# Performance work log

Measured on AMD Instinct MI355X. Metric: run time of the kernel, lower is better.

Reference implementation:

```python
import jax, jax.numpy as jnp
import numpy as np

N, E, KS, DIM = 6890, 41340, 5, 2
K = KS * KS  # 25 spline kernel buckets


def spline_conv(x, edge_index, pseudo, weight, root, bias):
    """Degree-1 open B-spline conv (SplineGCN), mean aggregation + root + bias.
    x: [N, Fin], weight: [K, Fin, Fout], root: [Fin, Fout], bias: [Fout]."""
    row, col = edge_index[0], edge_index[1]  # target, source
    pos = pseudo * (KS - 1)                   # [E, 2] in [0, KS-1]
    i0 = jnp.clip(jnp.floor(pos), 0, KS - 2).astype(jnp.int32)  # [E, 2]
    frac = pos - i0                           # [E, 2]
    # 4 nonzero basis products per edge (2 per dim)
    off = jnp.array([[0, 0], [1, 0], [0, 1], [1, 1]], dtype=jnp.int32)  # [4, 2]
    b_dim = jnp.stack([1.0 - frac, frac], axis=-1)  # [E, 2, 2] (dim, which-knot)
    w = b_dim[:, 0, off[:, 0]] * b_dim[:, 1, off[:, 1]]       # [E, 4]
    idx = (i0[:, None, 0] + off[None, :, 0]) + KS * (i0[:, None, 1] + off[None, :, 1])  # [E, 4]
    # transform all nodes by all K kernels once: [N, K, Fout]
    xw = jnp.einsum('ni,kio->nko', x, weight)
    g = xw[col[:, None], idx]                 # [E, 4, Fout] gather
    msg = jnp.einsum('es,eso->eo', w, g)      # [E, Fout]
    agg = jax.ops.segment_sum(msg, row, num_segments=N)
    deg = jax.ops.segment_sum(jnp.ones((E,), x.dtype), row, num_segments=N)
    agg = agg / jnp.maximum(deg, 1.0)[:, None]
    return agg + x @ root + bias


def setup_inputs() -> dict:
    key = jax.random.key(0)
    ks = jax.random.split(key, 20)
    def gl(k, shape):  # glorot-ish
        fan = shape[-2] if len(shape) > 1 else shape[-1]
        return jax.random.normal(k, shape, jnp.float32) / np.sqrt(fan)
    inp = {
        'x': jax.random.normal(ks[0], (N, 544), jnp.float32),
        'edge_index': jax.random.randint(ks[1], (2, E), 0, N),
        'pseudo': jax.random.uniform(ks[2], (E, DIM), jnp.float32),
        'W_lin': gl(ks[3], (544, 16)), 'b_lin': jnp.zeros((16,), jnp.float32),
        'w1': gl(ks[4], (K, 16, 32)),  'r1': gl(ks[5], (16, 32)),  'bi1': jnp.zeros((32,), jnp.float32),
        'w2': gl(ks[6], (K, 32, 64)),  'r2': gl(ks[7], (32, 64)),  'bi2': jnp.zeros((64,), jnp.float32),
        'w3': gl(ks[8], (K, 64, 128)), 'r3': gl(ks[9], (64, 128)), 'bi3': jnp.zeros((128,), jnp.float32),
        'W1': gl(ks[10], (128, 256)), 'b1': jnp.zeros((256,), jnp.float32),
        'W2': gl(ks[11], (256, 6890)), 'b2': jnp.zeros((6890,), jnp.float32),
    }
    return inp


def reference(x, edge_index, pseudo, W_lin, b_lin, w1, r1, bi1, w2, r2, bi2, w3, r3, bi3, W1, b1, W2, b2):
    h = jax.nn.elu(x @ W_lin + b_lin)
    h = jax.nn.elu(spline_conv(h, edge_index, pseudo, w1, r1, bi1))
    h = jax.nn.elu(spline_conv(h, edge_index, pseudo, w2, r2, bi2))
    h = jax.nn.elu(spline_conv(h, edge_index, pseudo, w3, r3, bi3))
    h = jax.nn.elu(h @ W1 + b1)
    # dropout is identity in eval mode
    logits = h @ W2 + b2
    return jax.nn.log_softmax(logits, axis=-1)
```

## Files before the change

kernel.cpp:

```cpp
#include <hip/hip_runtime.h>
#include <hip/hip_bf16.h>

#define NND 6890
#define NED 41340

typedef __bf16 bf16x8 __attribute__((ext_vector_type(8)));
typedef float f32x4 __attribute__((ext_vector_type(4)));
typedef unsigned short u16x4 __attribute__((ext_vector_type(4)));

__device__ inline unsigned short f32_bf16(float f) {
  unsigned int u = __float_as_uint(f);
  unsigned int r = (u + 0x7FFFu + ((u >> 16) & 1u)) >> 16;
  return (unsigned short)r;
}
__device__ inline void split2(float v, unsigned short& hi, unsigned short& lo) {
  unsigned short h = f32_bf16(v);
  float hf = __uint_as_float((unsigned int)h << 16);
  hi = h;
  lo = f32_bf16(v - hf);
}
__device__ inline float elu_f(float v) { return v > 0.f ? v : (expf(v) - 1.f); }

__device__ __forceinline__ void gload_lds16(const void* g, void* l) {
  __builtin_amdgcn_global_load_lds((const __attribute__((address_space(1))) void*)g,
                                   (__attribute__((address_space(3))) void*)l, 16, 0, 0);
}

__global__ void zero_int_kernel(int* p, int n) {
  int i = blockIdx.x * blockDim.x + threadIdx.x;
  if (i < n) p[i] = 0;
}

__global__ void edge_prep_kernel(const int* __restrict__ erow, const float* __restrict__ pseudo,
                                 float* __restrict__ ew, int* __restrict__ ek,
                                 int* __restrict__ deg, int E) {
  int e = blockIdx.x * blockDim.x + threadIdx.x;
  if (e >= E) return;
  float p0 = pseudo[2 * e + 0] * 4.0f;
  float p1 = pseudo[2 * e + 1] * 4.0f;
  int i0 = (int)floorf(p0); i0 = i0 < 0 ? 0 : (i0 > 3 ? 3 : i0);
  int i1 = (int)floorf(p1); i1 = i1 < 0 ? 0 : (i1 > 3 ? 3 : i1);
  float f0 = p0 - (float)i0, f1 = p1 - (float)i1;
  ew[4 * e + 0] = (1.f - f0) * (1.f - f1);
  ew[4 * e + 1] = f0 * (1.f - f1);
  ew[4 * e + 2] = (1.f - f0) * f1;
  ew[4 * e + 3] = f0 * f1;
  int b = i0 + 5 * i1;
  ek[4 * e + 0] = b; ek[4 * e + 1] = b + 1; ek[4 * e + 2] = b + 5; ek[4 * e + 3] = b + 6;
  atomicAdd(&deg[erow[e]], 1);
}

__global__ void scan_kernel(const int* __restrict__ deg, int* __restrict__ rowptr,
                            int* __restrict__ cursor, float* __restrict__ deginv, int n) {
  __shared__ int part[1024];
  int t = threadIdx.x;
  int CH = (n + 1023) >> 10;
  int base = t * CH;
  int s = 0;
  for (int j = 0; j < CH; ++j) { int i = base + j; if (i < n) s += deg[i]; }
  part[t] = s;
  __syncthreads();
  for (int off = 1; off < 1024; off <<= 1) {
    int v = (t >= off) ? part[t - off] : 0;
    __syncthreads();
    part[t] += v;
    __syncthreads();
  }
  int run = (t == 0) ? 0 : part[t - 1];
  for (int j = 0; j < CH; ++j) {
    int i = base + j;
    if (i < n) {
      rowptr[i] = run; cursor[i] = run;
      int d = deg[i];
      deginv[i] = 1.0f / fmaxf((float)d, 1.0f);
      run += d;
    }
  }
  if (t == 1023) rowptr[n] = part[1023];
}

__global__ void csr_fill_kernel(const int* __restrict__ erow, int* __restrict__ cursor,
                                int* __restrict__ csr, int E) {
  int e = blockIdx.x * blockDim.x + threadIdx.x;
  if (e >= E) return;
  int slot = atomicAdd(&cursor[erow[e]], 1);
  csr[slot] = e;
}

__global__ void split_kernel(const float* __restrict__ src, unsigned short* __restrict__ oh,
                             unsigned short* __restrict__ ol, int n4) {
  int i = blockIdx.x * 256 + threadIdx.x;
  if (i >= n4) return;
  f32x4 v = *(const f32x4*)(src + 4 * i);
  u16x4 h, l;
#pragma unroll
  for (int j = 0; j < 4; ++j) {
    unsigned short hh, ll;
    split2(v[j], hh, ll);
    h[j] = hh; l[j] = ll;
  }
  *(u16x4*)(oh + 4 * i) = h;
  *(u16x4*)(ol + 4 * i) = l;
}

__global__ void b_build_kernel(const float* __restrict__ x, const int* __restrict__ ecol,
                               const float* __restrict__ ew4, const int* __restrict__ ek4,
                               const int* __restrict__ rowptr, const int* __restrict__ csr,
                               const float* __restrict__ deginv,
                               unsigned short* __restrict__ Bh, unsigned short* __restrict__ Bl,
                               int Fin) {
  extern __shared__ float lds[];
  int r = blockIdx.x;
  int T = blockDim.x;
  int tid = threadIdx.x;
  int nb = 25 * Fin;
  int j = tid / Fin;
  int i = tid - j * Fin;
  float* plane = lds + j * nb;
  for (int t = tid; t < 4 * nb; t += T) lds[t] = 0.f;
  __syncthreads();
  int p0 = rowptr[r], p1 = rowptr[r + 1];
  for (int p = p0 + j; p < p1; p += 4) {
    int e = csr[p];
    int c = ecol[e];
    float xv = x[(size_t)c * Fin + i];
    f32x4 wv = *(const f32x4*)(ew4 + 4 * e);
    int4 kv = *(const int4*)(ek4 + 4 * e);
    plane[kv.x * Fin + i] += wv[0] * xv;
    plane[kv.y * Fin + i] += wv[1] * xv;
    plane[kv.z * Fin + i] += wv[2] * xv;
    plane[kv.w * Fin + i] += wv[3] * xv;
  }
  __syncthreads();
  float dinv = deginv[r];
  int tot = nb + Fin;
  for (int t = tid; t < tot; t += T) {
    float v;
    if (t < nb)
      v = (lds[t] + lds[nb + t] + lds[2 * nb + t] + lds[3 * nb + t]) * dinv;
    else
      v = x[(size_t)r * Fin + (t - nb)];
    unsigned short h, l;
    split2(v, h, l);
    Bh[(size_t)r * tot + t] = h;
    Bl[(size_t)r * tot + t] = l;
  }
}

__global__ void weights_prep_kernel(const float* __restrict__ W_lin, const float* __restrict__ w1,
                                    const float* __restrict__ r1, const float* __restrict__ w2,
                                    const float* __restrict__ r2, const float* __restrict__ w3,
                                    const float* __restrict__ r3, const float* __restrict__ W1,
                                    unsigned short* __restrict__ Th, unsigned short* __restrict__ Tl) {
  const int tstart[9] = {0, 17, 30, 31, 81, 83, 283, 291, 323};
  const int jK[8]    = {544, 400, 16, 800, 32, 1600, 64, 128};
  const int jF[8]    = {16, 32, 32, 64, 64, 128, 128, 256};
  const int jldt[8]  = {544, 416, 416, 832, 832, 1664, 1664, 128};
  const int jkoff[8] = {0, 0, 400, 0, 800, 0, 1600, 0};
  const int jdst[8]  = {0, 8704, 8704, 22016, 22016, 75264, 75264, 288256};
  int b = blockIdx.x;
  int job = 0;
  while (job < 7 && b >= tstart[job + 1]) ++job;
  int t = b - tstart[job];
  int fxc = (jF[job] + 31) >> 5;
  int kt = t / fxc, ft = t % fxc;
  const float* src;
  switch (job) {
    case 0: src = W_lin; break;
    case 1: src = w1; break;
    case 2: src = r1; break;
    case 3: src = w2; break;
    case 4: src = r2; break;
    case 5: src = w3; break;
    case 6: src = r3; break;
    default: src = W1; break;
  }
  int K = jK[job], F = jF[job], ldt = jldt[job], koff = jkoff[job];
  unsigned short* th = Th + jdst[job];
  unsigned short* tl = Tl + jdst[job];
  int k0 = kt * 32, c0 = ft * 32;
  __shared__ float tbuf[32][33];
  int tx = threadIdx.x & 31, ty = threadIdx.x >> 5;
  for (int j = ty; j < 32; j += 8) {
    int gk = k0 + j, gc = c0 + tx;
    tbuf[j][tx] = (gk < K && gc < F) ? src[(size_t)gk * F + gc] : 0.f;
  }
  __syncthreads();
  for (int j = ty; j < 32; j += 8) {
    int gc = c0 + j, gk = k0 + tx;
    if (gc < F && gk < K) {
      unsigned short h, lo2;
      split2(tbuf[tx][j], h, lo2);
      th[(size_t)gc * ldt + koff + gk] = h;
      tl[(size_t)gc * ldt + koff + gk] = lo2;
    }
  }
}

template <int BN>
__global__ __launch_bounds__(256) void gemm_x3_partial_kernel(
    const unsigned short* __restrict__ Ah, const unsigned short* __restrict__ Al,
    const unsigned short* __restrict__ Wh, const unsigned short* __restrict__ Wl,
    float* __restrict__ P, int M, int Kd, int F, int KS) {
  constexpr int AE = 64 * 32;
  constexpr int WE = BN * 32;
  __shared__ __align__(16) unsigned short lds[2][2 * AE + 2 * WE];
  int tid = threadIdx.x;
  int wave = tid >> 6, lane = tid & 63;
  int g = lane >> 4, r = lane & 15;
  int row0 = blockIdx.y * 64;
  int col0 = blockIdx.x * BN;
  int z = blockIdx.z;
  int nt = Kd >> 5;
  int ta = z * nt / KS, tb = (z + 1) * nt / KS;

  auto STAGE = [&](int buf, int kb) {
    {
      int rr = tid >> 2, pos = tid & 3;
      int c = (pos - rr) & 3;
      int gra = row0 + rr; if (gra >= M) gra = M - 1;
      size_t so = (size_t)gra * Kd + kb + c * 8;
      gload_lds16(Ah + so, &lds[buf][wave * 512]);
      gload_lds16(Al + so, &lds[buf][AE + wave * 512]);
    }
#pragma unroll
    for (int it = 0; it < (4 * BN + 255) / 256; ++it) {
      int idx = it * 256 + tid;
      if (idx < 4 * BN) {
        int rr = idx >> 2, pos = idx & 3;
        int c = (pos - rr) & 3;
        size_t so = (size_t)(col0 + rr) * Kd + kb + c * 8;
        gload_lds16(Wh + so, &lds[buf][2 * AE + (it * 256 + wave * 64) * 8]);
        gload_lds16(Wl + so, &lds[buf][2 * AE + WE + (it * 256 + wave * 64) * 8]);
      }
    }
  };

  constexpr int NF = BN / 16;
  f32x4 acc[NF];
#pragma unroll
  for (int n = 0; n < NF; ++n)
#pragma unroll
    for (int q = 0; q < 4; ++q) acc[n][q] = 0.f;

  int n = tb - ta;
  int rA = wave * 16 + r;
  int aoff = rA * 32 + ((g + rA) & 3) * 8;

  STAGE(0, ta * 32);
  __syncthreads();
  for (int tt = 0; tt < n; ++tt) {
    int buf = tt & 1;
    if (tt + 1 < n) STAGE(buf ^ 1, (ta + tt + 1) * 32);
    bf16x8 fah = *(const bf16x8*)&lds[buf][aoff];
    bf16x8 fal = *(const bf16x8*)&lds[buf][AE + aoff];
#pragma unroll
    for (int nn = 0; nn < NF; ++nn) {
      int rW = nn * 16 + r;
      int woff = rW * 32 + ((g + rW) & 3) * 8;
      bf16x8 fbh = *(const bf16x8*)&lds[buf][2 * AE + woff];
      bf16x8 fbl = *(const bf16x8*)&lds[buf][2 * AE + WE + woff];
      acc[nn] = __builtin_amdgcn_mfma_f32_16x16x32_bf16(fah, fbh, acc[nn], 0, 0, 0);
      acc[nn] = __builtin_amdgcn_mfma_f32_16x16x32_bf16(fal, fbh, acc[nn], 0, 0, 0);
      acc[nn] = __builtin_amdgcn_mfma_f32_16x16x32_bf16(fah, fbl, acc[nn], 0, 0, 0);
    }
    __syncthreads();
  }
#pragma unroll
  for (int nn = 0; nn < NF; ++nn) {
    int gc = col0 + nn * 16 + r;
#pragma unroll
    for (int q = 0; q < 4; ++q) {
      int gr = row0 + wave * 16 + g * 4 + q;
      if (gr < M) P[((size_t)z * M + gr) * F + gc] = acc[nn][q];
    }
  }
}

__global__ __launch_bounds__(256) void combine_elu_kernel(
    const float* __restrict__ P, const float* __restrict__ bias,
    float* __restrict__ outF, unsigned short* __restrict__ outB,
    unsigned short* __restrict__ outH, unsigned short* __restrict__ outL,
    int M, int F, int KS) {
  int i4 = blockIdx.x * 256 + threadIdx.x;
  int fv = F >> 2;
  int total = M * fv;
  if (i4 >= total) return;
  int gr = i4 / fv, c4 = (i4 - gr * fv) * 4;
  f32x4 s = {0.f, 0.f, 0.f, 0.f};
  for (int z = 0; z < KS; ++z)
    s += *(const f32x4*)(P + ((size_t)z * M + gr) * F + c4);
  f32x4 bv = *(const f32x4*)(bias + c4);
#pragma unroll
  for (int j = 0; j < 4; ++j) s[j] = elu_f(s[j] + bv[j]);
  if (outH) {
    u16x4 h, l;
#pragma unroll
    for (int j = 0; j < 4; ++j) {
      unsigned short hh, ll;
      split2(s[j], hh, ll);
      h[j] = hh; l[j] = ll;
    }
    *(u16x4*)(outH + (size_t)gr * F + c4) = h;
    *(u16x4*)(outL + (size_t)gr * F + c4) = l;
  } else if (outB) {
    u16x4 o;
#pragma unroll
    for (int j = 0; j < 4; ++j) o[j] = f32_bf16(s[j]);
    *(u16x4*)(outB + (size_t)gr * F + c4) = o;
  } else {
    *(f32x4*)(outF + (size_t)gr * F + c4) = s;
  }
}

__global__ void w2_cast_transpose_kernel(const float* __restrict__ W2,
                                         unsigned short* __restrict__ Wt, int K, int N) {
  __shared__ float t[32][33];
  int c0 = blockIdx.x * 32, k0 = blockIdx.y * 32;
  int tx = threadIdx.x, ty = threadIdx.y;
  for (int j = ty; j < 32; j += 8) {
    int gk = k0 + j, gc = c0 + tx;
    t[j][tx] = (gk < K && gc < N) ? W2[(size_t)gk * N + gc] : 0.f;
  }
  __syncthreads();
  for (int j = ty; j < 32; j += 8) {
    int gc = c0 + j, gk = k0 + tx;
    if (gc < N && gk < K) Wt[(size_t)gc * K + gk] = f32_bf16(t[tx][j]);
  }
}

template <int MODE>
__global__ __launch_bounds__(256) void gemm_final_kernel(
    const unsigned short* __restrict__ A, const unsigned short* __restrict__ Bt,
    const float* __restrict__ bias, const float* __restrict__ lse,
    float* __restrict__ outp, int M, int N) {
  __shared__ __align__(16) unsigned short lds[2][2][8192];
  int tid = threadIdx.x;
  int w = tid >> 6, l = tid & 63;
  int row0 = blockIdx.y * 128, col0 = blockIdx.x * 128;

  auto STAGE = [&](int buf, int kb) {
#pragma unroll
    for (int it = 0; it < 4; ++it) {
      int idx = it * 256 + tid;
      int rr = idx >> 3, pos = idx & 7;
      int c = (pos - rr) & 7;
      int gra = row0 + rr; if (gra >= M) gra = M - 1;
      int grb = col0 + rr; if (grb >= N) grb = N - 1;
      gload_lds16(A + (size_t)gra * 256 + kb + c * 8, &lds[buf][0][(it * 256 + w * 64) * 8]);
      gload_lds16(Bt + (size_t)grb * 256 + kb + c * 8, &lds[buf][1][(it * 256 + w * 64) * 8]);
    }
  };

  int wm = w >> 1, wn = w & 1;
  int g = l >> 4, r = l & 15;

  f32x4 acc[4][4];
#pragma unroll
  for (int mi = 0; mi < 4; ++mi)
#pragma unroll
    for (int ni = 0; ni < 4; ++ni)
#pragma unroll
      for (int q = 0; q < 4; ++q) acc[mi][ni][q] = 0.f;

  STAGE(0, 0);
  __syncthreads();
#pragma unroll
  for (int ks = 0; ks < 4; ++ks) {
    int buf = ks & 1;
    if (ks < 3) STAGE(buf ^ 1, (ks + 1) * 64);
#pragma unroll
    for (int sub = 0; sub < 2; ++sub) {
      bf16x8 fa[4], fb[4];
#pragma unroll
      for (int mi = 0; mi < 4; ++mi) {
        int rA = wm * 64 + mi * 16 + r;
        fa[mi] = *(const bf16x8*)&lds[buf][0][rA * 64 + ((g + 4 * sub + rA) & 7) * 8];
      }
#pragma unroll
      for (int ni = 0; ni < 4; ++ni) {
        int rB = wn * 64 + ni * 16 + r;
        fb[ni] = *(const bf16x8*)&lds[buf][1][rB * 64 + ((g + 4 * sub + rB) & 7) * 8];
      }
#pragma unroll
      for (int mi = 0; mi < 4; ++mi)
#pragma unroll
        for (int ni = 0; ni < 4; ++ni)
          acc[mi][ni] = __builtin_amdgcn_mfma_f32_16x16x32_bf16(fb[ni], fa[mi], acc[mi][ni], 0, 0, 0);
    }
    __syncthreads();
  }

  if (MODE == 0) {
    float bb[4][4];
#pragma unroll
    for (int ni = 0; ni < 4; ++ni) {
      int gc0 = col0 + wn * 64 + ni * 16 + g * 4;
#pragma unroll
      for (int q = 0; q < 4; ++q)
        bb[ni][q] = (gc0 + q < N) ? bias[gc0 + q] : 0.f;
    }
#pragma unroll
    for (int mi = 0; mi < 4; ++mi) {
      int gr = row0 + wm * 64 + mi * 16 + r;
      float vv[4][4];
      float mloc = -3e38f;
#pragma unroll
      for (int ni = 0; ni < 4; ++ni) {
        int gc0 = col0 + wn * 64 + ni * 16 + g * 4;
#pragma unroll
        for (int q = 0; q < 4; ++q) {
          float v = (gc0 + q < N) ? (acc[mi][ni][q] + bb[ni][q]) : -3e38f;
          vv[ni][q] = v;
          mloc = fmaxf(mloc, v);
        }
      }
      float sloc = 0.f;
#pragma unroll
      for (int ni = 0; ni < 4; ++ni) {
        int gc0 = col0 + wn * 64 + ni * 16 + g * 4;
#pragma unroll
        for (int q = 0; q < 4; ++q)
          if (gc0 + q < N) sloc += __expf(vv[ni][q] - mloc);
      }
#pragma unroll
      for (int off = 16; off < 64; off <<= 1) {
        float mo = __shfl_xor(mloc, off);
        float so = __shfl_xor(sloc, off);
        float mn = fmaxf(mloc, mo);
        sloc = sloc * __expf(mloc - mn) + so * __expf(mo - mn);
        mloc = mn;
      }
      if (g == 0 && gr < M) {
        int hb = blockIdx.x * 2 + wn;
        *(float2*)(outp + 2 * ((size_t)hb * M + gr)) = make_float2(mloc, sloc);
      }
    }
  } else {
    float* fsc = (float*)&lds[0][0][0];
    float* wbase = fsc + w * 4096;
#pragma unroll
    for (int mi = 0; mi < 4; ++mi) {
      int rr = mi * 16 + r;
#pragma unroll
      for (int ni = 0; ni < 4; ++ni) {
        int u = (ni * 4 + g + rr) & 15;
        *(f32x4*)(wbase + rr * 64 + u * 4) = acc[mi][ni];
      }
    }
    __syncthreads();
#pragma unroll
    for (int t = 0; t < 16; ++t) {
      int unit = t * 256 + tid;
      int rowi = unit >> 5, ch = unit & 31;
      int gr = row0 + rowi;
      if (gr >= M) continue;
      int reg = ((rowi >> 6) << 1) + (ch >> 4);
      int rr = rowi & 63;
      int u = ((ch & 15) + rr) & 15;
      f32x4 v = *(const f32x4*)(fsc + reg * 4096 + rr * 64 + u * 4);
      float L = lse[gr];
      int gc0 = col0 + ch * 4;
      if (gc0 + 4 <= N) {
        f32x4 bv = *(const f32x4*)(bias + gc0);
#pragma unroll
        for (int q = 0; q < 4; ++q) v[q] = v[q] + bv[q] - L;
        *(f32x4*)(outp + (size_t)gr * N + gc0) = v;
      } else {
#pragma unroll
        for (int q = 0; q < 4; ++q)
          if (gc0 + q < N) outp[(size_t)gr * N + gc0 + q] = v[q] + bias[gc0 + q] - L;
      }
    }
  }
}

__global__ __launch_bounds__(256) void lse_kernel(const float* __restrict__ stats,
                                                  float* __restrict__ lse, int M, int NH) {
  int row = blockIdx.x * 256 + threadIdx.x;
  if (row >= M) return;
  float m = -3e38f, s = 0.f;
  for (int hb = 0; hb < NH; ++hb) {
    float2 v = *(const float2*)(stats + 2 * ((size_t)hb * M + row));
    float mn = fmaxf(m, v.x);
    s = s * __expf(m - mn) + v.y * __expf(v.x - mn);
    m = mn;
  }
  lse[row] = m + logf(s);
}

extern "C" void kernel_launch(void* const* d_in, const int* in_sizes, int n_in,
                              void* d_out, int out_size, void* d_ws, size_t ws_size,
                              hipStream_t stream) {
  const int N = NND, E = NED;
  const float* x      = (const float*)d_in[0];
  const int*   ei     = (const int*)d_in[1];
  const float* pseudo = (const float*)d_in[2];
  const float* W_lin  = (const float*)d_in[3];
  const float* b_lin  = (const float*)d_in[4];
  const float* w1  = (const float*)d_in[5];
  const float* r1  = (const float*)d_in[6];
  const float* bi1 = (const float*)d_in[7];
  const float* w2  = (const float*)d_in[8];
  const float* r2  = (const float*)d_in[9];
  const float* bi2 = (const float*)d_in[10];
  const float* w3  = (const float*)d_in[11];
  const float* r3  = (const float*)d_in[12];
  const float* bi3 = (const float*)d_in[13];
  const float* W1  = (const float*)d_in[14];
  const float* b1  = (const float*)d_in[15];
  const float* W2  = (const float*)d_in[16];
  const float* b2  = (const float*)d_in[17];
  const int* erow = ei;
  const int* ecol = ei + E;

  char* scratch = (char*)d_out;
  size_t off = 0;
  auto alloc = [&](size_t bytes) -> void* {
    void* p = scratch + off;
    off = (off + bytes + 255) & ~(size_t)255;
    return p;
  };
  unsigned short* Bh = (unsigned short*)alloc((size_t)N * 1664 * 2);
  unsigned short* Bl = (unsigned short*)alloc((size_t)N * 1664 * 2);
  float* h0     = (float*)alloc((size_t)N * 16 * 4);
  float* h1     = (float*)alloc((size_t)N * 32 * 4);
  float* h2     = (float*)alloc((size_t)N * 64 * 4);
  unsigned short* h3h = (unsigned short*)alloc((size_t)N * 128 * 2);
  unsigned short* h3l = (unsigned short*)alloc((size_t)N * 128 * 2);
  unsigned short* xh  = (unsigned short*)alloc((size_t)N * 544 * 2);
  unsigned short* xl  = (unsigned short*)alloc((size_t)N * 544 * 2);
  unsigned short* Wth = (unsigned short*)alloc((size_t)321024 * 2);
  unsigned short* Wtl = (unsigned short*)alloc((size_t)321024 * 2);
  float* Pbuf   = (float*)alloc((size_t)4 * N * 128 * 4);
  float* stats  = (float*)alloc((size_t)108 * N * 2 * 4);
  float* ew     = (float*)alloc((size_t)E * 4 * 4);
  int*   ek     = (int*)alloc((size_t)E * 4 * 4);
  int*   deg    = (int*)alloc((size_t)N * 4);
  float* deginv = (float*)alloc((size_t)N * 4);
  int*   rowptr = (int*)alloc((size_t)(N + 1) * 4);
  int*   cursor = (int*)alloc((size_t)N * 4);
  int*   csr    = (int*)alloc((size_t)E * 4);

  unsigned short* h4b = (unsigned short*)d_ws;
  unsigned short* W2t = (unsigned short*)((char*)d_ws + (size_t)N * 256 * 2);
  float* lse = (float*)((char*)d_ws + (size_t)N * 256 * 4);

  zero_int_kernel<<<(N + 255) / 256, 256, 0, stream>>>(deg, N);
  edge_prep_kernel<<<(E + 255) / 256, 256, 0, stream>>>(erow, pseudo, ew, ek, deg, E);
  scan_kernel<<<1, 1024, 0, stream>>>(deg, rowptr, cursor, deginv, N);
  csr_fill_kernel<<<(E + 255) / 256, 256, 0, stream>>>(erow, cursor, csr, E);

  weights_prep_kernel<<<323, 256, 0, stream>>>(W_lin, w1, r1, w2, r2, w3, r3, W1, Wth, Wtl);
  split_kernel<<<(N * 136 + 255) / 256, 256, 0, stream>>>(x, xh, xl, N * 136);

  auto cgrid = [](int M_, int F_) { return dim3((M_ * (F_ / 4) + 255) / 256); };

  gemm_x3_partial_kernel<16><<<dim3(1, 108, 4), 256, 0, stream>>>(xh, xl, Wth + 0, Wtl + 0, Pbuf, N, 544, 16, 4);
  combine_elu_kernel<<<cgrid(N, 16), 256, 0, stream>>>(Pbuf, b_lin, h0, nullptr, nullptr, nullptr, N, 16, 4);

  b_build_kernel<<<N, 64, 4 * 25 * 16 * 4, stream>>>(h0, ecol, ew, ek, rowptr, csr, deginv, Bh, Bl, 16);
  gemm_x3_partial_kernel<32><<<dim3(1, 108, 4), 256, 0, stream>>>(Bh, Bl, Wth + 8704, Wtl + 8704, Pbuf, N, 416, 32, 4);
  combine_elu_kernel<<<cgrid(N, 32), 256, 0, stream>>>(Pbuf, bi1, h1, nullptr, nullptr, nullptr, N, 32, 4);

  b_build_kernel<<<N, 128, 4 * 25 * 32 * 4, stream>>>(h1, ecol, ew, ek, rowptr, csr, deginv, Bh, Bl, 32);
  gemm_x3_partial_kernel<64><<<dim3(1, 108, 4), 256, 0, stream>>>(Bh, Bl, Wth + 22016, Wtl + 22016, Pbuf, N, 832, 64, 4);
  combine_elu_kernel<<<cgrid(N, 64), 256, 0, stream>>>(Pbuf, bi2, h2, nullptr, nullptr, nullptr, N, 64, 4);

  b_build_kernel<<<N, 256, 4 * 25 * 64 * 4, stream>>>(h2, ecol, ew, ek, rowptr, csr, deginv, Bh, Bl, 64);
  gemm_x3_partial_kernel<128><<<dim3(1, 108, 4), 256, 0, stream>>>(Bh, Bl, Wth + 75264, Wtl + 75264, Pbuf, N, 1664, 128, 4);
  combine_elu_kernel<<<cgrid(N, 128), 256, 0, stream>>>(Pbuf, bi3, nullptr, nullptr, h3h, h3l, N, 128, 4);

  gemm_x3_partial_kernel<128><<<dim3(2, 108, 2), 256, 0, stream>>>(h3h, h3l, Wth + 288256, Wtl + 288256, Pbuf, N, 128, 256, 2);
  combine_elu_kernel<<<cgrid(N, 256), 256, 0, stream>>>(Pbuf, b1, nullptr, h4b, nullptr, nullptr, N, 256, 2);

  w2_cast_transpose_kernel<<<dim3(216, 8), dim3(32, 8), 0, stream>>>(W2, W2t, 256, N);

  gemm_final_kernel<0><<<dim3(54, 54), 256, 0, stream>>>(h4b, W2t, b2, nullptr, stats, N, N);

  lse_kernel<<<(N + 255) / 256, 256, 0, stream>>>(stats, lse, N, 108);

  gemm_final_kernel<1><<<dim3(54, 54), 256, 0, stream>>>(h4b, W2t, b2, lse, (float*)d_out, N, N);

  (void)in_sizes; (void)n_in; (void)out_size; (void)ws_size;
}
```

Before: 315.5 us.

## Fuse bias+ELU epilogue into GEMMs, drop split-K, merge prep kernels

Removes the split-K partial-sum buffer and the separate combine_elu kernels. Each GEMM now uses 32-row tiles with 128 threads, runs the full K loop, and applies bias, ELU and the output conversion in its epilogue. The weight, x-split and W2 transpose prep kernels are merged into one launch, and the zeroing kernel becomes a memset. This cuts launch count and the partial-sum traffic, but each block now carries the whole K reduction with fewer waves, which lowers per-block parallelism on the larger layers.

```diff
diff --git a/kernel.cpp b/kernel.cpp
--- a/kernel.cpp
+++ b/kernel.cpp
@@ -24,11 +24,6 @@
 __device__ __forceinline__ void gload_lds16(const void* g, void* l) {
   __builtin_amdgcn_global_load_lds((const __attribute__((address_space(1))) void*)g,
                                    (__attribute__((address_space(3))) void*)l, 16, 0, 0);
-}
-
-__global__ void zero_int_kernel(int* p, int n) {
-  int i = blockIdx.x * blockDim.x + threadIdx.x;
-  if (i < n) p[i] = 0;
 }
 
 __global__ void edge_prep_kernel(const int* __restrict__ erow, const float* __restrict__ pseudo,
@@ -87,20 +82,88 @@
   csr[slot] = e;
 }
 
-__global__ void split_kernel(const float* __restrict__ src, unsigned short* __restrict__ oh,
-                             unsigned short* __restrict__ ol, int n4) {
-  int i = blockIdx.x * 256 + threadIdx.x;
-  if (i >= n4) return;
-  f32x4 v = *(const f32x4*)(src + 4 * i);
-  u16x4 h, l;
-#pragma unroll
-  for (int j = 0; j < 4; ++j) {
-    unsigned short hh, ll;
-    split2(v[j], hh, ll);
-    h[j] = hh; l[j] = ll;
-  }
-  *(u16x4*)(oh + 4 * i) = h;
-  *(u16x4*)(ol + 4 * i) = l;
+__global__ void prep_all_kernel(const float* __restrict__ W_lin, const float* __restrict__ w1,
+                                const float* __restrict__ r1, const float* __restrict__ w2,
+                                const float* __restrict__ r2, const float* __restrict__ w3,
+                                const float* __restrict__ r3, const float* __restrict__ W1,
+                                const float* __restrict__ x, const float* __restrict__ W2,
+                                unsigned short* __restrict__ Th, unsigned short* __restrict__ Tl,
+                                unsigned short* __restrict__ xh, unsigned short* __restrict__ xl,
+                                unsigned short* __restrict__ W2t) {
+  int b = blockIdx.x;
+  int tid = threadIdx.x;
+  if (b < 323) {
+    const int tstart[9] = {0, 17, 30, 31, 81, 83, 283, 291, 323};
+    const int jK[8]    = {544, 400, 16, 800, 32, 1600, 64, 128};
+    const int jF[8]    = {16, 32, 32, 64, 64, 128, 128, 256};
+    const int jldt[8]  = {544, 416, 416, 832, 832, 1664, 1664, 128};
+    const int jkoff[8] = {0, 0, 400, 0, 800, 0, 1600, 0};
+    const int jdst[8]  = {0, 8704, 8704, 22016, 22016, 75264, 75264, 288256};
+    int job = 0;
+    while (job < 7 && b >= tstart[job + 1]) ++job;
+    int t = b - tstart[job];
+    int fxc = (jF[job] + 31) >> 5;
+    int kt = t / fxc, ft = t % fxc;
+    const float* src;
+    switch (job) {
+      case 0: src = W_lin; break;
+      case 1: src = w1; break;
+      case 2: src = r1; break;
+      case 3: src = w2; break;
+      case 4: src = r2; break;
+      case 5: src = w3; break;
+      case 6: src = r3; break;
+      default: src = W1; break;
+    }
+    int K = jK[job], F = jF[job], ldt = jldt[job], koff = jkoff[job];
+    unsigned short* th = Th + jdst[job];
+    unsigned short* tl = Tl + jdst[job];
+    int k0 = kt * 32, c0 = ft * 32;
+    __shared__ float tbuf[32][33];
+    int tx = tid & 31, ty = tid >> 5;
+    for (int j = ty; j < 32; j += 8) {
+      int gk = k0 + j, gc = c0 + tx;
+      tbuf[j][tx] = (gk < K && gc < F) ? src[(size_t)gk * F + gc] : 0.f;
+    }
+    __syncthreads();
+    for (int j = ty; j < 32; j += 8) {
+      int gc = c0 + j, gk = k0 + tx;
+      if (gc < F && gk < K) {
+        unsigned short h, lo2;
+        split2(tbuf[tx][j], h, lo2);
+        th[(size_t)gc * ldt + koff + gk] = h;
+        tl[(size_t)gc * ldt + koff + gk] = lo2;
+      }
+    }
+  } else if (b < 3984) {
+    int i = (b - 323) * 256 + tid;
+    if (i < NND * 136) {
+      f32x4 v = *(const f32x4*)(x + 4 * (size_t)i);
+      u16x4 h, l;
+#pragma unroll
+      for (int j = 0; j < 4; ++j) {
+        unsigned short hh, ll;
+        split2(v[j], hh, ll);
+        h[j] = hh; l[j] = ll;
+      }
+      *(u16x4*)(xh + 4 * (size_t)i) = h;
+      *(u16x4*)(xl + 4 * (size_t)i) = l;
+    }
+  } else {
+    int t = b - 3984;
+    int c0 = (t % 216) * 32, k0 = (t / 216) * 32;
+    __shared__ float tb2[32][33];
+    int tx = tid & 31, ty = tid >> 5;
+    for (int j = ty; j < 32; j += 8) {
+      int gk = k0 + j, gc = c0 + tx;
+      tb2[j][tx] = (gk < 256 && gc < NND) ? W2[(size_t)gk * NND + gc] : 0.f;
+    }
+    __syncthreads();
+    for (int j = ty; j < 32; j += 8) {
+      int gc = c0 + j, gk = k0 + tx;
+      if (gc < NND && gk < 256) W2t[(size_t)gc * 256 + gk] = f32_bf16(tb2[tx][j]);
+    }
+  }
 }
 
 __global__ void b_build_kernel(const float* __restrict__ x, const int* __restrict__ ecol,
@@ -147,72 +210,24 @@
   }
 }
 
-__global__ void weights_prep_kernel(const float* __restrict__ W_lin, const float* __restrict__ w1,
-                                    const float* __restrict__ r1, const float* __restrict__ w2,
-                                    const float* __restrict__ r2, const float* __restrict__ w3,
-                                    const float* __restrict__ r3, const float* __restrict__ W1,
-                                    unsigned short* __restrict__ Th, unsigned short* __restrict__ Tl) {
-  const int tstart[9] = {0, 17, 30, 31, 81, 83, 283, 291, 323};
-  const int jK[8]    = {544, 400, 16, 800, 32, 1600, 64, 128};
-  const int jF[8]    = {16, 32, 32, 64, 64, 128, 128, 256};
-  const int jldt[8]  = {544, 416, 416, 832, 832, 1664, 1664, 128};
-  const int jkoff[8] = {0, 0, 400, 0, 800, 0, 1600, 0};
-  const int jdst[8]  = {0, 8704, 8704, 22016, 22016, 75264, 75264, 288256};
-  int b = blockIdx.x;
-  int job = 0;
-  while (job < 7 && b >= tstart[job + 1]) ++job;
-  int t = b - tstart[job];
-  int fxc = (jF[job] + 31) >> 5;
-  int kt = t / fxc, ft = t % fxc;
-  const float* src;
-  switch (job) {
-    case 0: src = W_lin; break;
-    case 1: src = w1; break;
-    case 2: src = r1; break;
-    case 3: src = w2; break;
-    case 4: src = r2; break;
-    case 5: src = w3; break;
-    case 6: src = r3; break;
-    default: src = W1; break;
-  }
-  int K = jK[job], F = jF[job], ldt = jldt[job], koff = jkoff[job];
-  unsigned short* th = Th + jdst[job];
-  unsigned short* tl = Tl + jdst[job];
-  int k0 = kt * 32, c0 = ft * 32;
-  __shared__ float tbuf[32][33];
-  int tx = threadIdx.x & 31, ty = threadIdx.x >> 5;
-  for (int j = ty; j < 32; j += 8) {
-    int gk = k0 + j, gc = c0 + tx;
-    tbuf[j][tx] = (gk < K && gc < F) ? src[(size_t)gk * F + gc] : 0.f;
-  }
-  __syncthreads();
-  for (int j = ty; j < 32; j += 8) {
-    int gc = c0 + j, gk = k0 + tx;
-    if (gc < F && gk < K) {
-      unsigned short h, lo2;
-      split2(tbuf[tx][j], h, lo2);
-      th[(size_t)gc * ldt + koff + gk] = h;
-      tl[(size_t)gc * ldt + koff + gk] = lo2;
-    }
-  }
-}
-
-template <int BN>
-__global__ __launch_bounds__(256) void gemm_x3_partial_kernel(
+template <int BN, int OM>
+__global__ __launch_bounds__(128) void gemm_x3_fused_kernel(
     const unsigned short* __restrict__ Ah, const unsigned short* __restrict__ Al,
     const unsigned short* __restrict__ Wh, const unsigned short* __restrict__ Wl,
-    float* __restrict__ P, int M, int Kd, int F, int KS) {
-  constexpr int AE = 64 * 32;
+    const float* __restrict__ bias, float* __restrict__ outF,
+    unsigned short* __restrict__ outH, unsigned short* __restrict__ outL,
+    unsigned short* __restrict__ outB, int M, int Kd, int F) {
+  constexpr int AE = 32 * 32;
   constexpr int WE = BN * 32;
+  constexpr int NF = BN / 16;
+  constexpr int WIT = (4 * BN + 127) / 128;
   __shared__ __align__(16) unsigned short lds[2][2 * AE + 2 * WE];
   int tid = threadIdx.x;
   int wave = tid >> 6, lane = tid & 63;
   int g = lane >> 4, r = lane & 15;
-  int row0 = blockIdx.y * 64;
+  int row0 = blockIdx.y * 32;
   int col0 = blockIdx.x * BN;
-  int z = blockIdx.z;
   int nt = Kd >> 5;
-  int ta = z * nt / KS, tb = (z + 1) * nt / KS;
 
   auto STAGE = [&](int buf, int kb) {
     {
@@ -224,34 +239,32 @@
       gload_lds16(Al + so, &lds[buf][AE + wave * 512]);
     }
 #pragma unroll
-    for (int it = 0; it < (4 * BN + 255) / 256; ++it) {
-      int idx = it * 256 + tid;
+    for (int it = 0; it < WIT; ++it) {
+      int idx = it * 128 + tid;
       if (idx < 4 * BN) {
         int rr = idx >> 2, pos = idx & 3;
         int c = (pos - rr) & 3;
         size_t so = (size_t)(col0 + rr) * Kd + kb + c * 8;
-        gload_lds16(Wh + so, &lds[buf][2 * AE + (it * 256 + wave * 64) * 8]);
-        gload_lds16(Wl + so, &lds[buf][2 * AE + WE + (it * 256 + wave * 64) * 8]);
+        gload_lds16(Wh + so, &lds[buf][2 * AE + (it * 128 + wave * 64) * 8]);
+        gload_lds16(Wl + so, &lds[buf][2 * AE + WE + (it * 128 + wave * 64) * 8]);
       }
     }
   };
 
-  constexpr int NF = BN / 16;
   f32x4 acc[NF];
 #pragma unroll
   for (int n = 0; n < NF; ++n)
 #pragma unroll
     for (int q = 0; q < 4; ++q) acc[n][q] = 0.f;
 
-  int n = tb - ta;
   int rA = wave * 16 + r;
   int aoff = rA * 32 + ((g + rA) & 3) * 8;
 
-  STAGE(0, ta * 32);
+  STAGE(0, 0);
   __syncthreads();
-  for (int tt = 0; tt < n; ++tt) {
+  for (int tt = 0; tt < nt; ++tt) {
     int buf = tt & 1;
-    if (tt + 1 < n) STAGE(buf ^ 1, (ta + tt + 1) * 32);
+    if (tt + 1 < nt) STAGE(buf ^ 1, (tt + 1) * 32);
     bf16x8 fah = *(const bf16x8*)&lds[buf][aoff];
     bf16x8 fal = *(const bf16x8*)&lds[buf][AE + aoff];
 #pragma unroll
@@ -269,63 +282,24 @@
 #pragma unroll
   for (int nn = 0; nn < NF; ++nn) {
     int gc = col0 + nn * 16 + r;
+    float bv = bias[gc];
 #pragma unroll
     for (int q = 0; q < 4; ++q) {
       int gr = row0 + wave * 16 + g * 4 + q;
-      if (gr < M) P[((size_t)z * M + gr) * F + gc] = acc[nn][q];
-    }
-  }
-}
-
-__global__ __launch_bounds__(256) void combine_elu_kernel(
-    const float* __restrict__ P, const float* __restrict__ bias,
-    float* __restrict__ outF, unsigned short* __restrict__ outB,
-    unsigned short* __restrict__ outH, unsigned short* __restrict__ outL,
-    int M, int F, int KS) {
-  int i4 = blockIdx.x * 256 + threadIdx.x;
-  int fv = F >> 2;
-  int total = M * fv;
-  if (i4 >= total) return;
-  int gr = i4 / fv, c4 = (i4 - gr * fv) * 4;
-  f32x4 s = {0.f, 0.f, 0.f, 0.f};
-  for (int z = 0; z < KS; ++z)
-    s += *(const f32x4*)(P + ((size_t)z * M + gr) * F + c4);
-  f32x4 bv = *(const f32x4*)(bias + c4);
-#pragma unroll
-  for (int j = 0; j < 4; ++j) s[j] = elu_f(s[j] + bv[j]);
-  if (outH) {
-    u16x4 h, l;
-#pragma unroll
-    for (int j = 0; j < 4; ++j) {
-      unsigned short hh, ll;
-      split2(s[j], hh, ll);
-      h[j] = hh; l[j] = ll;
-    }
-    *(u16x4*)(outH + (size_t)gr * F + c4) = h;
-    *(u16x4*)(outL + (size_t)gr * F + c4) = l;
-  } else if (outB) {
-    u16x4 o;
-#pragma unroll
-    for (int j = 0; j < 4; ++j) o[j] = f32_bf16(s[j]);
-    *(u16x4*)(outB + (size_t)gr * F + c4) = o;
-  } else {
-    *(f32x4*)(outF + (size_t)gr * F + c4) = s;
-  }
-}
-
-__global__ void w2_cast_transpose_kernel(const float* __restrict__ W2,
-                                         unsigned short* __restrict__ Wt, int K, int N) {
-  __shared__ float t[32][33];
-  int c0 = blockIdx.x * 32, k0 = blockIdx.y * 32;
-  int tx = threadIdx.x, ty = threadIdx.y;
-  for (int j = ty; j < 32; j += 8) {
-    int gk = k0 + j, gc = c0 + tx;
-    t[j][tx] = (gk < K && gc < N) ? W2[(size_t)gk * N + gc] : 0.f;
-  }
-  __syncthreads();
-  for (int j = ty; j < 32; j += 8) {
-    int gc = c0 + j, gk = k0 + tx;
-    if (gc < N && gk < K) Wt[(size_t)gc * K + gk] = f32_bf16(t[tx][j]);
+      if (gr < M) {
+        float v = elu_f(acc[nn][q] + bv);
+        if (OM == 0) {
+          outF[(size_t)gr * F + gc] = v;
+        } else if (OM == 1) {
+          unsigned short h, l;
+          split2(v, h, l);
+          outH[(size_t)gr * F + gc] = h;
+          outL[(size_t)gr * F + gc] = l;
+        } else {
+          outB[(size_t)gr * F + gc] = f32_bf16(v);
+        }
+      }
+    }
   }
 }
 
@@ -532,7 +506,6 @@
   unsigned short* xl  = (unsigned short*)alloc((size_t)N * 544 * 2);
   unsigned short* Wth = (unsigned short*)alloc((size_t)321024 * 2);
   unsigned short* Wtl = (unsigned short*)alloc((size_t)321024 * 2);
-  float* Pbuf   = (float*)alloc((size_t)4 * N * 128 * 4);
   float* stats  = (float*)alloc((size_t)108 * N * 2 * 4);
   float* ew     = (float*)alloc((size_t)E * 4 * 4);
   int*   ek     = (int*)alloc((size_t)E * 4 * 4);
@@ -546,35 +519,33 @@
   unsigned short* W2t = (unsigned short*)((char*)d_ws + (size_t)N * 256 * 2);
   float* lse = (float*)((char*)d_ws + (size_t)N * 256 * 4);
 
-  zero_int_kernel<<<(N + 255) / 256, 256, 0, stream>>>(deg, N);
+  hipMemsetAsync(deg, 0, (size_t)N * 4, stream);
   edge_prep_kernel<<<(E + 255) / 256, 256, 0, stream>>>(erow, pseudo, ew, ek, deg, E);
   scan_kernel<<<1, 1024, 0, stream>>>(deg, rowptr, cursor, deginv, N);
   csr_fill_kernel<<<(E + 255) / 256, 256, 0, stream>>>(erow, cursor, csr, E);
 
-  weights_prep_kernel<<<323, 256, 0, stream>>>(W_lin, w1, r1, w2, r2, w3, r3, W1, Wth, Wtl);
-  split_kernel<<<(N * 136 + 255) / 256, 256, 0, stream>>>(x, xh, xl, N * 136);
-
-  auto cgrid = [](int M_, int F_) { return dim3((M_ * (F_ / 4) + 255) / 256); };
-
-  gemm_x3_partial_kernel<16><<<dim3(1, 108, 4), 256, 0, stream>>>(xh, xl, Wth + 0, Wtl + 0, Pbuf, N, 544, 16, 4);
-  combine_elu_kernel<<<cgrid(N, 16), 256, 0, stream>>>(Pbuf, b_lin, h0, nullptr, nullptr, nullptr, N, 16, 4);
+  prep_all_kernel<<<5712, 256, 0, stream>>>(W_lin, w1, r1, w2, r2, w3, r3, W1, x, W2,
+                                            Wth, Wtl, xh, xl, W2t);
+
+  const int GY = (N + 31) / 32;
+
+  gemm_x3_fused_kernel<16, 0><<<dim3(1, GY), 128, 0, stream>>>(
+      xh, xl, Wth + 0, Wtl + 0, b_lin, h0, nullptr, nullptr, nullptr, N, 544, 16);
 
   b_build_kernel<<<N, 64, 4 * 25 * 16 * 4, stream>>>(h0, ecol, ew, ek, rowptr, csr, deginv, Bh, Bl, 16);
-  gemm_x3_partial_kernel<32><<<dim3(1, 108, 4), 256, 0, stream>>>(Bh, Bl, Wth + 8704, Wtl + 8704, Pbuf, N, 416, 32, 4);
-  combine_elu_kernel<<<cgrid(N, 32), 256, 0, stream>>>(Pbuf, bi1, h1, nullptr, nullptr, nullptr, N, 32, 4);
+  gemm_x3_fused_kernel<32, 0><<<dim3(1, GY), 128, 0, stream>>>(
+      Bh, Bl, Wth + 8704, Wtl + 8704, bi1, h1, nullptr, nullptr, nullptr, N, 416, 32);
 
   b_build_kernel<<<N, 128, 4 * 25 * 32 * 4, stream>>>(h1, ecol, ew, ek, rowptr, csr, deginv, Bh, Bl, 32);
-  gemm_x3_partial_kernel<64><<<dim3(1, 108, 4), 256, 0, stream>>>(Bh, Bl, Wth + 22016, Wtl + 22016, Pbuf, N, 832, 64, 4);
-  combine_elu_kernel<<<cgrid(N, 64), 256, 0, stream>>>(Pbuf, bi2, h2, nullptr, nullptr, nullptr, N, 64, 4);
+  gemm_x3_fused_kernel<64, 0><<<dim3(1, GY), 128, 0, stream>>>(
+      Bh, Bl, Wth + 22016, Wtl + 22016, bi2, h2, nullptr, nullptr, nullptr, N, 832, 64);
 
   b_build_kernel<<<N, 256, 4 * 25 * 64 * 4, stream>>>(h2, ecol, ew, ek, rowptr, csr, deginv, Bh, Bl, 64);
-  gemm_x3_partial_kernel<128><<<dim3(1, 108, 4), 256, 0, stream>>>(Bh, Bl, Wth + 75264, Wtl + 75264, Pbuf, N, 1664, 128, 4);
-  combine_elu_kernel<<<cgrid(N, 128), 256, 0, stream>>>(Pbuf, bi3, nullptr, nullptr, h3h, h3l, N, 128, 4);
-
-  gemm_x3_partial_kernel<128><<<dim3(2, 108, 2), 256, 0, stream>>>(h3h, h3l, Wth + 288256, Wtl + 288256, Pbuf, N, 128, 256, 2);
-  combine_elu_kernel<<<cgrid(N, 256), 256, 0, stream>>>(Pbuf, b1, nullptr, h4b, nullptr, nullptr, N, 256, 2);
-
-  w2_cast_transpose_kernel<<<dim3(216, 8), dim3(32, 8), 0, stream>>>(W2, W2t, 256, N);
+  gemm_x3_fused_kernel<128, 1><<<dim3(1, GY), 128, 0, stream>>>(
+      Bh, Bl, Wth + 75264, Wtl + 75264, bi3, nullptr, h3h, h3l, nullptr, N, 1664, 128);
+
+  gemm_x3_fused_kernel<128, 2><<<dim3(2, GY), 128, 0, stream>>>(
+      h3h, h3l, Wth + 288256, Wtl + 288256, b1, nullptr, nullptr, nullptr, h4b, N, 128, 256);
 
   gemm_final_kernel<0><<<dim3(54, 54), 256, 0, stream>>>(h4b, W2t, b2, nullptr, stats, N, N);
 
```

After: 339.9 us. 1.08x slower.
